# Kernel tuning notes

Measured on AMD Instinct MI355X. Metric: run time of the kernel, lower is better.

The kernel has to match this reference:

```python
import jax, jax.numpy as jnp
import numpy as np

N_NODES = 50000
N_EDGES = 600000
IN_CH, HID1, HID2, OUT_CH = 128, 256, 128, 2


def setup_inputs() -> dict:
    key = jax.random.key(0)
    ks = jax.random.split(key, 8)
    x = jax.random.normal(ks[0], (N_NODES, IN_CH), dtype=jnp.float32)
    edge_index = jax.random.randint(ks[1], (2, N_EDGES), 0, N_NODES, dtype=jnp.int64)
    # Glorot-style init for GCN linear weights
    def glorot(k, fan_in, fan_out):
        s = jnp.sqrt(6.0 / (fan_in + fan_out)).astype(jnp.float32)
        return jax.random.uniform(k, (fan_in, fan_out), jnp.float32, -s, s)
    return {
        "x": x,
        "W1": glorot(ks[2], IN_CH, HID1), "b1": jnp.zeros((HID1,), jnp.float32),
        "W2": glorot(ks[3], HID1, HID2), "b2": jnp.zeros((HID2,), jnp.float32),
        "W3": glorot(ks[4], HID2, OUT_CH), "b3": jnp.zeros((OUT_CH,), jnp.float32),
        "edge_index": edge_index,
    }


def _gcn_graph(edge_index, n_nodes):
    # Add self-loops (GCNConv default) and compute symmetric normalization
    loop = jnp.arange(n_nodes, dtype=edge_index.dtype)
    src = jnp.concatenate([edge_index[0], loop])
    dst = jnp.concatenate([edge_index[1], loop])
    ones = jnp.ones(src.shape[0], dtype=jnp.float32)
    deg = jax.ops.segment_sum(ones, dst, num_segments=n_nodes)
    dinv = jnp.where(deg > 0, jax.lax.rsqrt(deg), 0.0)
    norm = dinv[src] * dinv[dst]  # [E + N]
    return src, dst, norm


def _gcn_layer(h, W, b, src, dst, norm, n_nodes):
    h = h @ W                                   # [N, d_out]
    msg = h[src] * norm[:, None]                # gather + scale  [E+N, d_out]
    agg = jax.ops.segment_sum(msg, dst, num_segments=n_nodes)
    return agg + b


def reference(x, W1, b1, W2, b2, W3, b3, edge_index):
    n = x.shape[0]
    src, dst, norm = _gcn_graph(edge_index, n)
    h = jax.nn.relu(_gcn_layer(x, W1, b1, src, dst, norm, n))
    # dropout p=0.5 is identity in eval mode (training=False)
    h = jax.nn.relu(_gcn_layer(h, W2, b2, src, dst, norm, n))
    h = _gcn_layer(h, W3, b3, src, dst, norm, n)
    return jax.nn.log_softmax(h, axis=1)
```

## Files before the change

kernel.cpp:

```cpp
#include <hip/hip_runtime.h>
#include <hip/hip_bf16.h>
#include <math.h>

#define N_NODES 50000
#define N_EDGES 600000
#define E_TOT   (N_EDGES + N_NODES)
#define M_PAD   50048
#define NODE_STRIDE 32
#define DUMMY_ROWS 65536
#define CSR_CAP (N_NODES * NODE_STRIDE + 2048)

typedef __attribute__((ext_vector_type(8))) short bf16x8;
typedef __attribute__((ext_vector_type(4))) float f32x4;
typedef __attribute__((ext_vector_type(2))) float f32x2;
typedef __attribute__((ext_vector_type(8))) unsigned short u16x8;


__device__ __forceinline__ unsigned short f2bf(float f) {
    unsigned int u = __float_as_uint(f);
    unsigned int r = (u + 0x7fffu + ((u >> 16) & 1u)) >> 16;
    return (unsigned short)r;
}

__device__ __forceinline__ void acc_row(f32x2* acc, uint4 v) {
    acc[0] += (f32x2){__uint_as_float(v.x << 16), __uint_as_float(v.x & 0xffff0000u)};
    acc[1] += (f32x2){__uint_as_float(v.y << 16), __uint_as_float(v.y & 0xffff0000u)};
    acc[2] += (f32x2){__uint_as_float(v.z << 16), __uint_as_float(v.z & 0xffff0000u)};
    acc[3] += (f32x2){__uint_as_float(v.w << 16), __uint_as_float(v.w & 0xffff0000u)};
}

#define GLD_LDS16(g, l) __builtin_amdgcn_global_load_lds( \
    (__attribute__((address_space(1))) void*)(void*)(g), \
    (__attribute__((address_space(3))) void*)(l), 16, 0, 0)


__global__ void prep_kernel(const int* __restrict__ ei, int* __restrict__ cnt,
                            const float* __restrict__ W1, const float* __restrict__ W2,
                            unsigned short* __restrict__ W1t, unsigned short* __restrict__ W2t,
                            unsigned short* __restrict__ csr, unsigned short* __restrict__ xs,
                            unsigned short* __restrict__ t2b, float2* __restrict__ Ts) {
    const int NB_S = (E_TOT + 255) / 256;
    int b = blockIdx.x;
    if (b < NB_S) {
        int e = b * 256 + threadIdx.x;
        if (e >= E_TOT) return;
        int s, d;
        if (e < N_EDGES) { s = ei[e]; d = ei[N_EDGES + e]; }
        else             { s = d = e - N_EDGES; }
        int slot = atomicAdd(&cnt[d], 1);
        if (slot < NODE_STRIDE)
            csr[d * NODE_STRIDE + slot] = (unsigned short)s;
    } else if (b < NB_S + 128) {
        int i = (b - NB_S) * 256 + threadIdx.x;
        int k = i >> 8, n = i & 255;
        W1t[(size_t)n * 128 + k] = f2bf(W1[i]);
    } else if (b < NB_S + 256) {
        int i = (b - NB_S - 128) * 256 + threadIdx.x;
        int k = i >> 7, n = i & 127;
        W2t[(size_t)n * 256 + k] = f2bf(W2[i]);
    } else {
        int t = threadIdx.x;
        if (t < 16)
            *(uint4*)(xs + (size_t)(DUMMY_ROWS - 1) * 128 + t * 8) = make_uint4(0, 0, 0, 0);
        else if (t < 32)
            *(uint4*)(t2b + (size_t)(DUMMY_ROWS - 1) * 128 + (t - 16) * 8) = make_uint4(0, 0, 0, 0);
        else if (t == 32)
            Ts[DUMMY_ROWS - 1] = make_float2(0.f, 0.f);
    }
}


__global__ void scale_kernel(const int* __restrict__ cnt, const float* __restrict__ x,
                             unsigned short* __restrict__ xs, float* __restrict__ dinv,
                             unsigned short* __restrict__ csr) {
    const int NB_C = (N_NODES * 32 + 255) / 256;
    int b = blockIdx.x;
    if (b < NB_C) {
        int i = b * 256 + threadIdx.x;
        if (i >= N_NODES * 32) return;
        float d = rsqrtf((float)cnt[i >> 5]);
        float4 v = *(const float4*)(x + (size_t)i * 4);
        ushort4 o;
        o.x = f2bf(v.x * d); o.y = f2bf(v.y * d); o.z = f2bf(v.z * d); o.w = f2bf(v.w * d);
        *(ushort4*)(xs + (size_t)i * 4) = o;
    } else {
        int i = (b - NB_C) * 256 + threadIdx.x;
        if (i < N_NODES) {
            int c = cnt[i];
            dinv[i] = rsqrtf((float)c);
            if (c > NODE_STRIDE) c = NODE_STRIDE;
            for (int s = c; s < NODE_STRIDE; ++s)
                csr[i * NODE_STRIDE + s] = 0xFFFFu;
        }
    }
}


__global__ __launch_bounds__(512, 6) void fused1_kernel(
    const unsigned short* __restrict__ Hs,
    const float* __restrict__ dinv,
    const int* __restrict__ cnt,
    const unsigned short* __restrict__ csr,
    const unsigned short* __restrict__ W1t,
    const unsigned short* __restrict__ W2t,
    const float* __restrict__ b1,
    unsigned short* __restrict__ C,
    int M) {
    __shared__ __align__(16) unsigned short smem[64 * 256 + 64 * 128];
    unsigned short* Atile = smem;
    unsigned short* h1buf = smem;
    unsigned short* Bs    = smem + 64 * 256;
    int tid = threadIdx.x;
    int lane = tid & 63;
    int m0 = blockIdx.x * 64;
    int mm = lane & 15, kg = lane >> 4;
    int rowg = (tid >> 6) & 3;
    int colg = tid >> 8;

    auto stage1 = [&](int n0) {
        #pragma unroll
        for (int it = 0; it < 2; ++it) {
            int ci = it * 512 + tid;
            int r = ci >> 4, c8 = (ci & 15) ^ (r & 15);
            const unsigned short* g = W1t + (size_t)(n0 + r) * 128 + c8 * 8;
            unsigned short* l = Bs + (size_t)(it * 512 + (tid & 448)) * 8;
            GLD_LDS16(g, l);
        }
    };
    auto stage2 = [&](int n0, int kh) {
        #pragma unroll
        for (int it = 0; it < 2; ++it) {
            int ci = it * 512 + tid;
            int r = ci >> 4, c8 = (ci & 15) ^ (r & 15);
            const unsigned short* g = W2t + (size_t)(n0 + r) * 256 + kh * 128 + c8 * 8;
            unsigned short* l = Bs + (size_t)(it * 512 + (tid & 448)) * 8;
            GLD_LDS16(g, l);
        }
    };

    stage1(0);

    {
        int q = tid & 15;
        int g = tid >> 4;
        #pragma unroll 1
        for (int pass = 0; pass < 2; ++pass) {
            int r = pass * 32 + g;
            int n = m0 + r;
            f32x2 acc2[4] = {};
            float dn = 0.f;
            if (n < N_NODES) {
                dn = dinv[n];
                int p = n * NODE_STRIDE;
                int pd = (cnt[n] + 3) & ~3;
                if (pd > NODE_STRIDE) pd = NODE_STRIDE;
                int pe = p + pd;
                ushort4 s4 = *(const ushort4*)(csr + p);
                while (p < pe) {
                    int pn = p + 4;
                    ushort4 nx = *(const ushort4*)(csr + pn);
                    uint4 v0 = *(const uint4*)(Hs + (size_t)s4.x * 128 + q * 8);
                    uint4 v1 = *(const uint4*)(Hs + (size_t)s4.y * 128 + q * 8);
                    uint4 v2 = *(const uint4*)(Hs + (size_t)s4.z * 128 + q * 8);
                    uint4 v3 = *(const uint4*)(Hs + (size_t)s4.w * 128 + q * 8);
                    acc_row(acc2, v0);
                    acc_row(acc2, v1);
                    acc_row(acc2, v2);
                    acc_row(acc2, v3);
                    p = pn; s4 = nx;
                }
            }
            float* acc = (float*)acc2;
            u16x8 ov;
            #pragma unroll
            for (int i2 = 0; i2 < 8; ++i2) ov[i2] = f2bf(acc[i2] * dn);
            *(u16x8*)(Atile + r * 128 + ((q ^ (r & 15)) * 8)) = ov;
        }
    }
    __syncthreads();

    bf16x8 aPre[4];
    #pragma unroll
    for (int kt = 0; kt < 4; ++kt) {
        int ml = rowg * 16 + mm;
        aPre[kt] = *(const bf16x8*)(Atile + ml * 128 + (((kt * 4 + kg) ^ mm) * 8));
    }
    __syncthreads();

    int bb[2];
    #pragma unroll
    for (int j = 0; j < 2; ++j) bb[j] = (colg * 32 + j * 16 + mm) * 128;
    int h1rd = (rowg * 16 + mm) * 256;

    #pragma unroll 1
    for (int nt = 0; nt < 4; ++nt) {
        int n0 = nt * 64;
        f32x4 acc[2];
        #pragma unroll
        for (int j = 0; j < 2; ++j) acc[j] = (f32x4){0.f, 0.f, 0.f, 0.f};
        #pragma unroll
        for (int kt = 0; kt < 4; ++kt) {
            bf16x8 bfr[2];
            #pragma unroll
            for (int j = 0; j < 2; ++j)
                bfr[j] = *(const bf16x8*)(Bs + bb[j] + (((kt * 4 + kg) ^ mm) * 8));
            #pragma unroll
            for (int j = 0; j < 2; ++j)
                acc[j] = __builtin_amdgcn_mfma_f32_16x16x32_bf16(aPre[kt], bfr[j], acc[j], 0, 0, 0);
        }
        float bj[2];
        #pragma unroll
        for (int j = 0; j < 2; ++j) bj[j] = b1[n0 + colg * 32 + j * 16 + mm];
        #pragma unroll
        for (int r = 0; r < 4; ++r) {
            int ml = rowg * 16 + kg * 4 + r;
            int rb = ml * 256, rx = ml & 15;
            #pragma unroll
            for (int j = 0; j < 2; ++j) {
                int c = n0 + colg * 32 + j * 16 + mm;
                int c8 = c >> 3;
                float v = fmaxf(acc[j][r] + bj[j], 0.f);
                h1buf[rb + ((c8 ^ rx) * 8) + (c & 7)] = f2bf(v);
            }
        }
        __syncthreads();
        if (nt < 3) {
            stage1((nt + 1) * 64);
            __syncthreads();
        }
    }

    stage2(0, 0);
    #pragma unroll 1
    for (int nh = 0; nh < 2; ++nh) {
        int n0 = nh * 64;
        f32x4 acc[2];
        #pragma unroll
        for (int j = 0; j < 2; ++j) acc[j] = (f32x4){0.f, 0.f, 0.f, 0.f};
        #pragma unroll 1
        for (int kh = 0; kh < 2; ++kh) {
            __syncthreads();
            #pragma unroll
            for (int kt = 0; kt < 4; ++kt) {
                bf16x8 af, bfr[2];
                int c8h = kh * 16 + kt * 4 + kg;
                af = *(const bf16x8*)(h1buf + h1rd + ((c8h ^ mm) * 8));
                #pragma unroll
                for (int j = 0; j < 2; ++j)
                    bfr[j] = *(const bf16x8*)(Bs + bb[j] + (((kt * 4 + kg) ^ mm) * 8));
                #pragma unroll
                for (int j = 0; j < 2; ++j)
                    acc[j] = __builtin_amdgcn_mfma_f32_16x16x32_bf16(af, bfr[j], acc[j], 0, 0, 0);
            }
            __syncthreads();
            int s = nh * 2 + kh + 1;
            if (s < 4) stage2((s >> 1) * 64, s & 1);
        }
        #pragma unroll
        for (int r = 0; r < 4; ++r) {
            int gm = m0 + rowg * 16 + kg * 4 + r;
            float sc = (gm < M) ? dinv[gm] : 0.f;
            #pragma unroll
            for (int j = 0; j < 2; ++j) {
                int gn = nh * 64 + colg * 32 + j * 16 + mm;
                C[(size_t)gm * 128 + gn] = f2bf(acc[j][r] * sc);
            }
        }
    }
}


__global__ __launch_bounds__(256) void agg2_kernel(
    const unsigned short* __restrict__ Hs,
    const float* __restrict__ dinv,
    const int* __restrict__ cnt, const unsigned short* __restrict__ csr,
    const float* __restrict__ b2, const float* __restrict__ W3,
    float2* __restrict__ Ts) {
    int wave = threadIdx.x >> 6;
    int lane = threadIdx.x & 63;
    int n = blockIdx.x * 4 + wave;
    if (n >= N_NODES) return;
    int quarter = lane >> 4;
    int q = lane & 15;
    f32x2 acc2[4] = {};
    int p0 = n * NODE_STRIDE;
    int pdeg = (cnt[n] + 15) & ~15;
    if (pdeg > NODE_STRIDE) pdeg = NODE_STRIDE;
    int pend = p0 + pdeg;
    int p = p0 + quarter * 4;
    ushort4 s4 = *(const ushort4*)(csr + p);
    while (p < pend) {
        int pn = p + 16;
        ushort4 n4 = *(const ushort4*)(csr + pn);
        uint4 v0 = *(const uint4*)(Hs + (size_t)s4.x * 128 + q * 8);
        uint4 v1 = *(const uint4*)(Hs + (size_t)s4.y * 128 + q * 8);
        uint4 v2 = *(const uint4*)(Hs + (size_t)s4.z * 128 + q * 8);
        uint4 v3 = *(const uint4*)(Hs + (size_t)s4.w * 128 + q * 8);
        acc_row(acc2, v0);
        acc_row(acc2, v1);
        acc_row(acc2, v2);
        acc_row(acc2, v3);
        p = pn; s4 = n4;
    }
    float* acc = (float*)acc2;
    #pragma unroll
    for (int i = 0; i < 8; ++i) {
        acc[i] += __shfl_xor(acc[i], 16);
        acc[i] += __shfl_xor(acc[i], 32);
    }
    float dn = dinv[n];
    float t0 = 0.f, t1 = 0.f;
    #pragma unroll
    for (int i = 0; i < 8; ++i) {
        int c = q * 8 + i;
        float h = fmaxf(acc[i] * dn + b2[c], 0.f);
        float2 w = ((const float2*)W3)[c];
        t0 += h * w.x; t1 += h * w.y;
    }
    #pragma unroll
    for (int off = 1; off < 16; off <<= 1) {
        t0 += __shfl_xor(t0, off);
        t1 += __shfl_xor(t1, off);
    }
    if (lane == 0) Ts[n] = make_float2(t0 * dn, t1 * dn);
}


__global__ void lsm_kernel(const float2* __restrict__ Ts, const float* __restrict__ dinv,
                           const int* __restrict__ cnt, const unsigned short* __restrict__ csr,
                           const float* __restrict__ b3, float* __restrict__ out) {
    int n = blockIdx.x * 256 + threadIdx.x;
    if (n >= N_NODES) return;
    float a0 = 0.f, a1 = 0.f;
    int p0 = n * NODE_STRIDE;
    int pdeg = (cnt[n] + 3) & ~3;
    if (pdeg > NODE_STRIDE) pdeg = NODE_STRIDE;
    int pend = p0 + pdeg;
    ushort4 s4 = *(const ushort4*)(csr + p0);
    for (int p = p0; p < pend; p += 4) {
        ushort4 n4 = *(const ushort4*)(csr + p + 4);
        float2 u0 = Ts[s4.x], u1 = Ts[s4.y], u2 = Ts[s4.z], u3 = Ts[s4.w];
        a0 += (u0.x + u1.x) + (u2.x + u3.x);
        a1 += (u0.y + u1.y) + (u2.y + u3.y);
        s4 = n4;
    }
    float dn = dinv[n];
    float v0 = a0 * dn + b3[0];
    float v1 = a1 * dn + b3[1];
    float m = fmaxf(v0, v1);
    float lse = m + logf(expf(v0 - m) + expf(v1 - m));
    out[n * 2 + 0] = v0 - lse;
    out[n * 2 + 1] = v1 - lse;
}


extern "C" void kernel_launch(void* const* d_in, const int* in_sizes, int n_in,
                              void* d_out, int out_size, void* d_ws, size_t ws_size,
                              hipStream_t stream) {
    const float* x  = (const float*)d_in[0];
    const float* W1 = (const float*)d_in[1];
    const float* b1 = (const float*)d_in[2];
    const float* W2 = (const float*)d_in[3];
    const float* b2 = (const float*)d_in[4];
    const float* W3 = (const float*)d_in[5];
    const float* b3 = (const float*)d_in[6];
    const int*   ei = (const int*)d_in[7];
    float* out = (float*)d_out;

    char* ws = (char*)d_ws;
    size_t off = 0;
    auto alloc = [&](size_t bytes) -> char* {
        char* p = ws + off;
        off = (off + bytes + 255) & ~(size_t)255;
        return p;
    };
    int*   cnt  = (int*)alloc(N_NODES * 4);
    float* dinv = (float*)alloc(N_NODES * 4);
    unsigned short* csr = (unsigned short*)alloc((size_t)CSR_CAP * 2);
    unsigned short* xs     = (unsigned short*)alloc((size_t)DUMMY_ROWS * 128 * 2);
    unsigned short* W1t    = (unsigned short*)alloc((size_t)256 * 128 * 2);
    unsigned short* W2t    = (unsigned short*)alloc((size_t)128 * 256 * 2);
    unsigned short* t2b    = (unsigned short*)alloc((size_t)DUMMY_ROWS * 128 * 2);
    float2* Ts = (float2*)alloc((size_t)DUMMY_ROWS * 8);

    hipMemsetAsync(cnt, 0, N_NODES * 4, stream);

    const int NB_S = (E_TOT + 255) / 256;
    prep_kernel<<<NB_S + 256 + 1, 256, 0, stream>>>(
        ei, cnt, W1, W2, W1t, W2t, csr, xs, t2b, Ts);

    const int NB_C = (N_NODES * 32 + 255) / 256;
    const int NB_D = (N_NODES + 255) / 256;
    scale_kernel<<<NB_C + NB_D, 256, 0, stream>>>(cnt, x, xs, dinv, csr);

    fused1_kernel<<<M_PAD / 64, 512, 0, stream>>>(
        xs, dinv, cnt, csr, W1t, W2t, b1, t2b, N_NODES);
    agg2_kernel<<<(N_NODES + 3) / 4, 256, 0, stream>>>(
        t2b, dinv, cnt, csr, b2, W3, Ts);

    lsm_kernel<<<(N_NODES + 255) / 256, 256, 0, stream>>>(Ts, dinv, cnt, csr, b3, out);
}
```

Baseline: 198.8 us.

## Fold scale kernel into prep by recomputing degree normalization on the fly

Removes the separate scale_kernel launch: x is converted to bf16 unscaled inside prep_kernel, and the dinv array and CSR padding fill are dropped. Consumers instead mask tail slots to a dummy zero row and compute rsqrt(cnt) where needed, including a per-neighbor source-degree weight in the first aggregation. This cuts one launch and one pass over x and the CSR, but adds an extra random cnt gather plus rsqrt per edge in fused1. The dummy row's cnt is set to 1 to keep that rsqrt finite.

```diff
diff --git a/kernel.cpp b/kernel.cpp
--- a/kernel.cpp
+++ b/kernel.cpp
@@ -29,6 +29,13 @@
     acc[3] += (f32x2){__uint_as_float(v.w << 16), __uint_as_float(v.w & 0xffff0000u)};
 }
 
+__device__ __forceinline__ void acc_row_s(f32x2* acc, uint4 v, float w) {
+    acc[0] += (f32x2){__uint_as_float(v.x << 16), __uint_as_float(v.x & 0xffff0000u)} * w;
+    acc[1] += (f32x2){__uint_as_float(v.y << 16), __uint_as_float(v.y & 0xffff0000u)} * w;
+    acc[2] += (f32x2){__uint_as_float(v.z << 16), __uint_as_float(v.z & 0xffff0000u)} * w;
+    acc[3] += (f32x2){__uint_as_float(v.w << 16), __uint_as_float(v.w & 0xffff0000u)} * w;
+}
+
 #define GLD_LDS16(g, l) __builtin_amdgcn_global_load_lds( \
     (__attribute__((address_space(1))) void*)(void*)(g), \
     (__attribute__((address_space(3))) void*)(l), 16, 0, 0)
@@ -36,10 +43,12 @@
 
 __global__ void prep_kernel(const int* __restrict__ ei, int* __restrict__ cnt,
                             const float* __restrict__ W1, const float* __restrict__ W2,
+                            const float* __restrict__ x,
                             unsigned short* __restrict__ W1t, unsigned short* __restrict__ W2t,
                             unsigned short* __restrict__ csr, unsigned short* __restrict__ xs,
                             unsigned short* __restrict__ t2b, float2* __restrict__ Ts) {
     const int NB_S = (E_TOT + 255) / 256;
+    const int NB_X = (N_NODES * 32 + 255) / 256;
     int b = blockIdx.x;
     if (b < NB_S) {
         int e = b * 256 + threadIdx.x;
@@ -58,6 +67,13 @@
         int i = (b - NB_S - 128) * 256 + threadIdx.x;
         int k = i >> 7, n = i & 127;
         W2t[(size_t)n * 256 + k] = f2bf(W2[i]);
+    } else if (b < NB_S + 256 + NB_X) {
+        int i = (b - NB_S - 256) * 256 + threadIdx.x;
+        if (i >= N_NODES * 32) return;
+        float4 v = *(const float4*)(x + (size_t)i * 4);
+        ushort4 o;
+        o.x = f2bf(v.x); o.y = f2bf(v.y); o.z = f2bf(v.z); o.w = f2bf(v.w);
+        *(ushort4*)(xs + (size_t)i * 4) = o;
     } else {
         int t = threadIdx.x;
         if (t < 16)
@@ -66,39 +82,14 @@
             *(uint4*)(t2b + (size_t)(DUMMY_ROWS - 1) * 128 + (t - 16) * 8) = make_uint4(0, 0, 0, 0);
         else if (t == 32)
             Ts[DUMMY_ROWS - 1] = make_float2(0.f, 0.f);
-    }
-}
-
-
-__global__ void scale_kernel(const int* __restrict__ cnt, const float* __restrict__ x,
-                             unsigned short* __restrict__ xs, float* __restrict__ dinv,
-                             unsigned short* __restrict__ csr) {
-    const int NB_C = (N_NODES * 32 + 255) / 256;
-    int b = blockIdx.x;
-    if (b < NB_C) {
-        int i = b * 256 + threadIdx.x;
-        if (i >= N_NODES * 32) return;
-        float d = rsqrtf((float)cnt[i >> 5]);
-        float4 v = *(const float4*)(x + (size_t)i * 4);
-        ushort4 o;
-        o.x = f2bf(v.x * d); o.y = f2bf(v.y * d); o.z = f2bf(v.z * d); o.w = f2bf(v.w * d);
-        *(ushort4*)(xs + (size_t)i * 4) = o;
-    } else {
-        int i = (b - NB_C) * 256 + threadIdx.x;
-        if (i < N_NODES) {
-            int c = cnt[i];
-            dinv[i] = rsqrtf((float)c);
-            if (c > NODE_STRIDE) c = NODE_STRIDE;
-            for (int s = c; s < NODE_STRIDE; ++s)
-                csr[i * NODE_STRIDE + s] = 0xFFFFu;
-        }
+        else if (t == 33)
+            cnt[DUMMY_ROWS - 1] = 1;
     }
 }
 
 
 __global__ __launch_bounds__(512, 6) void fused1_kernel(
     const unsigned short* __restrict__ Hs,
-    const float* __restrict__ dinv,
     const int* __restrict__ cnt,
     const unsigned short* __restrict__ csr,
     const unsigned short* __restrict__ W1t,
@@ -150,24 +141,32 @@
             f32x2 acc2[4] = {};
             float dn = 0.f;
             if (n < N_NODES) {
-                dn = dinv[n];
-                int p = n * NODE_STRIDE;
-                int pd = (cnt[n] + 3) & ~3;
+                int cn = cnt[n];
+                dn = rsqrtf((float)cn);
+                int pd = (cn + 3) & ~3;
                 if (pd > NODE_STRIDE) pd = NODE_STRIDE;
-                int pe = p + pd;
-                ushort4 s4 = *(const ushort4*)(csr + p);
-                while (p < pe) {
-                    int pn = p + 4;
-                    ushort4 nx = *(const ushort4*)(csr + pn);
-                    uint4 v0 = *(const uint4*)(Hs + (size_t)s4.x * 128 + q * 8);
-                    uint4 v1 = *(const uint4*)(Hs + (size_t)s4.y * 128 + q * 8);
-                    uint4 v2 = *(const uint4*)(Hs + (size_t)s4.z * 128 + q * 8);
-                    uint4 v3 = *(const uint4*)(Hs + (size_t)s4.w * 128 + q * 8);
-                    acc_row(acc2, v0);
-                    acc_row(acc2, v1);
-                    acc_row(acc2, v2);
-                    acc_row(acc2, v3);
-                    p = pn; s4 = nx;
+                const unsigned short* cp = csr + n * NODE_STRIDE;
+                ushort4 s4 = *(const ushort4*)cp;
+                #pragma unroll 1
+                for (int rel = 0; rel < pd; rel += 4) {
+                    ushort4 nx = *(const ushort4*)(cp + rel + 4);
+                    int i0 = (rel + 0 < cn) ? (int)s4.x : (DUMMY_ROWS - 1);
+                    int i1 = (rel + 1 < cn) ? (int)s4.y : (DUMMY_ROWS - 1);
+                    int i2 = (rel + 2 < cn) ? (int)s4.z : (DUMMY_ROWS - 1);
+                    int i3 = (rel + 3 < cn) ? (int)s4.w : (DUMMY_ROWS - 1);
+                    uint4 v0 = *(const uint4*)(Hs + (size_t)i0 * 128 + q * 8);
+                    uint4 v1 = *(const uint4*)(Hs + (size_t)i1 * 128 + q * 8);
+                    uint4 v2 = *(const uint4*)(Hs + (size_t)i2 * 128 + q * 8);
+                    uint4 v3 = *(const uint4*)(Hs + (size_t)i3 * 128 + q * 8);
+                    float w0 = rsqrtf((float)cnt[i0]);
+                    float w1 = rsqrtf((float)cnt[i1]);
+                    float w2 = rsqrtf((float)cnt[i2]);
+                    float w3 = rsqrtf((float)cnt[i3]);
+                    acc_row_s(acc2, v0, w0);
+                    acc_row_s(acc2, v1, w1);
+                    acc_row_s(acc2, v2, w2);
+                    acc_row_s(acc2, v3, w3);
+                    s4 = nx;
                 }
             }
             float* acc = (float*)acc2;
@@ -233,7 +232,6 @@
     stage2(0, 0);
     #pragma unroll 1
     for (int nh = 0; nh < 2; ++nh) {
-        int n0 = nh * 64;
         f32x4 acc[2];
         #pragma unroll
         for (int j = 0; j < 2; ++j) acc[j] = (f32x4){0.f, 0.f, 0.f, 0.f};
@@ -259,7 +257,8 @@
         #pragma unroll
         for (int r = 0; r < 4; ++r) {
             int gm = m0 + rowg * 16 + kg * 4 + r;
-            float sc = (gm < M) ? dinv[gm] : 0.f;
+            float sc = 0.f;
+            if (gm < M) sc = rsqrtf((float)cnt[gm]);
             #pragma unroll
             for (int j = 0; j < 2; ++j) {
                 int gn = nh * 64 + colg * 32 + j * 16 + mm;
@@ -272,7 +271,6 @@
 
 __global__ __launch_bounds__(256) void agg2_kernel(
     const unsigned short* __restrict__ Hs,
-    const float* __restrict__ dinv,
     const int* __restrict__ cnt, const unsigned short* __restrict__ csr,
     const float* __restrict__ b2, const float* __restrict__ W3,
     float2* __restrict__ Ts) {
@@ -283,24 +281,27 @@
     int quarter = lane >> 4;
     int q = lane & 15;
     f32x2 acc2[4] = {};
-    int p0 = n * NODE_STRIDE;
-    int pdeg = (cnt[n] + 15) & ~15;
+    int cn = cnt[n];
+    int pdeg = (cn + 15) & ~15;
     if (pdeg > NODE_STRIDE) pdeg = NODE_STRIDE;
-    int pend = p0 + pdeg;
-    int p = p0 + quarter * 4;
-    ushort4 s4 = *(const ushort4*)(csr + p);
-    while (p < pend) {
-        int pn = p + 16;
-        ushort4 n4 = *(const ushort4*)(csr + pn);
-        uint4 v0 = *(const uint4*)(Hs + (size_t)s4.x * 128 + q * 8);
-        uint4 v1 = *(const uint4*)(Hs + (size_t)s4.y * 128 + q * 8);
-        uint4 v2 = *(const uint4*)(Hs + (size_t)s4.z * 128 + q * 8);
-        uint4 v3 = *(const uint4*)(Hs + (size_t)s4.w * 128 + q * 8);
+    const unsigned short* cp = csr + n * NODE_STRIDE;
+    int rel = quarter * 4;
+    ushort4 s4 = *(const ushort4*)(cp + rel);
+    while (rel < pdeg) {
+        ushort4 n4 = *(const ushort4*)(cp + rel + 16);
+        int i0 = (rel + 0 < cn) ? (int)s4.x : (DUMMY_ROWS - 1);
+        int i1 = (rel + 1 < cn) ? (int)s4.y : (DUMMY_ROWS - 1);
+        int i2 = (rel + 2 < cn) ? (int)s4.z : (DUMMY_ROWS - 1);
+        int i3 = (rel + 3 < cn) ? (int)s4.w : (DUMMY_ROWS - 1);
+        uint4 v0 = *(const uint4*)(Hs + (size_t)i0 * 128 + q * 8);
+        uint4 v1 = *(const uint4*)(Hs + (size_t)i1 * 128 + q * 8);
+        uint4 v2 = *(const uint4*)(Hs + (size_t)i2 * 128 + q * 8);
+        uint4 v3 = *(const uint4*)(Hs + (size_t)i3 * 128 + q * 8);
         acc_row(acc2, v0);
         acc_row(acc2, v1);
         acc_row(acc2, v2);
         acc_row(acc2, v3);
-        p = pn; s4 = n4;
+        rel += 16; s4 = n4;
     }
     float* acc = (float*)acc2;
     #pragma unroll
@@ -308,7 +309,7 @@
         acc[i] += __shfl_xor(acc[i], 16);
         acc[i] += __shfl_xor(acc[i], 32);
     }
-    float dn = dinv[n];
+    float dn = rsqrtf((float)cn);
     float t0 = 0.f, t1 = 0.f;
     #pragma unroll
     for (int i = 0; i < 8; ++i) {
@@ -326,25 +327,29 @@
 }
 
 
-__global__ void lsm_kernel(const float2* __restrict__ Ts, const float* __restrict__ dinv,
+__global__ void lsm_kernel(const float2* __restrict__ Ts,
                            const int* __restrict__ cnt, const unsigned short* __restrict__ csr,
                            const float* __restrict__ b3, float* __restrict__ out) {
     int n = blockIdx.x * 256 + threadIdx.x;
     if (n >= N_NODES) return;
     float a0 = 0.f, a1 = 0.f;
-    int p0 = n * NODE_STRIDE;
-    int pdeg = (cnt[n] + 3) & ~3;
+    int cn = cnt[n];
+    int pdeg = (cn + 3) & ~3;
     if (pdeg > NODE_STRIDE) pdeg = NODE_STRIDE;
-    int pend = p0 + pdeg;
-    ushort4 s4 = *(const ushort4*)(csr + p0);
-    for (int p = p0; p < pend; p += 4) {
-        ushort4 n4 = *(const ushort4*)(csr + p + 4);
-        float2 u0 = Ts[s4.x], u1 = Ts[s4.y], u2 = Ts[s4.z], u3 = Ts[s4.w];
+    const unsigned short* cp = csr + n * NODE_STRIDE;
+    ushort4 s4 = *(const ushort4*)cp;
+    for (int rel = 0; rel < pdeg; rel += 4) {
+        ushort4 n4 = *(const ushort4*)(cp + rel + 4);
+        int i0 = (rel + 0 < cn) ? (int)s4.x : (DUMMY_ROWS - 1);
+        int i1 = (rel + 1 < cn) ? (int)s4.y : (DUMMY_ROWS - 1);
+        int i2 = (rel + 2 < cn) ? (int)s4.z : (DUMMY_ROWS - 1);
+        int i3 = (rel + 3 < cn) ? (int)s4.w : (DUMMY_ROWS - 1);
+        float2 u0 = Ts[i0], u1 = Ts[i1], u2 = Ts[i2], u3 = Ts[i3];
         a0 += (u0.x + u1.x) + (u2.x + u3.x);
         a1 += (u0.y + u1.y) + (u2.y + u3.y);
         s4 = n4;
     }
-    float dn = dinv[n];
+    float dn = rsqrtf((float)cn);
     float v0 = a0 * dn + b3[0];
     float v1 = a1 * dn + b3[1];
     float m = fmaxf(v0, v1);
@@ -374,8 +379,7 @@
         off = (off + bytes + 255) & ~(size_t)255;
         return p;
     };
-    int*   cnt  = (int*)alloc(N_NODES * 4);
-    float* dinv = (float*)alloc(N_NODES * 4);
+    int*   cnt  = (int*)alloc((size_t)DUMMY_ROWS * 4);
     unsigned short* csr = (unsigned short*)alloc((size_t)CSR_CAP * 2);
     unsigned short* xs     = (unsigned short*)alloc((size_t)DUMMY_ROWS * 128 * 2);
     unsigned short* W1t    = (unsigned short*)alloc((size_t)256 * 128 * 2);
@@ -383,20 +387,17 @@
     unsigned short* t2b    = (unsigned short*)alloc((size_t)DUMMY_ROWS * 128 * 2);
     float2* Ts = (float2*)alloc((size_t)DUMMY_ROWS * 8);
 
-    hipMemsetAsync(cnt, 0, N_NODES * 4, stream);
+    hipMemsetAsync(cnt, 0, (size_t)DUMMY_ROWS * 4, stream);
 
     const int NB_S = (E_TOT + 255) / 256;
-    prep_kernel<<<NB_S + 256 + 1, 256, 0, stream>>>(
-        ei, cnt, W1, W2, W1t, W2t, csr, xs, t2b, Ts);
-
-    const int NB_C = (N_NODES * 32 + 255) / 256;
-    const int NB_D = (N_NODES + 255) / 256;
-    scale_kernel<<<NB_C + NB_D, 256, 0, stream>>>(cnt, x, xs, dinv, csr);
+    const int NB_X = (N_NODES * 32 + 255) / 256;
+    prep_kernel<<<NB_S + 256 + NB_X + 1, 256, 0, stream>>>(
+        ei, cnt, W1, W2, x, W1t, W2t, csr, xs, t2b, Ts);
 
     fused1_kernel<<<M_PAD / 64, 512, 0, stream>>>(
-        xs, dinv, cnt, csr, W1t, W2t, b1, t2b, N_NODES);
+        xs, cnt, csr, W1t, W2t, b1, t2b, N_NODES);
     agg2_kernel<<<(N_NODES + 3) / 4, 256, 0, stream>>>(
-        t2b, dinv, cnt, csr, b2, W3, Ts);
-
-    lsm_kernel<<<(N_NODES + 255) / 256, 256, 0, stream>>>(Ts, dinv, cnt, csr, b3, out);
-}
+        t2b, cnt, csr, b2, W3, Ts);
+
+    lsm_kernel<<<(N_NODES + 255) / 256, 256, 0, stream>>>(Ts, cnt, csr, b3, out);
+}
```

Measured after the change: 195.3 us. About the same (-1.7%).
